# Kernel tuning notes

Hardware: AMD Instinct MI355X
Metric: run time of the kernel (lower is better)

## Reference

```python
import jax, jax.numpy as jnp
import numpy as np
import math

D = 1024
H = 16
FF = 4096
BS = 4
N = 1024
NEG_INF = -jnp.inf


def layer_norm(x, g, b, eps=1e-5):
    mu = jnp.mean(x, axis=-1, keepdims=True)
    var = jnp.var(x, axis=-1, keepdims=True)
    return (x - mu) * jax.lax.rsqrt(var + eps) * g + b


def mha(x, kv, Wq, Wk, Wv, g, b, causal):
    bs, n, d = x.shape
    n_kv = kv.shape[1]
    hd = d // H
    q = (x @ Wq).reshape(bs, n, H, hd)
    k = (kv @ Wk).reshape(bs, n_kv, H, hd)
    v = (kv @ Wv).reshape(bs, n_kv, H, hd)
    # scores scaled by 1/sqrt(model_dim) as in the original (not head_dim!)
    scores = jnp.einsum('bihd,bjhd->bhij', q, k) / math.sqrt(d)
    if causal:
        i = jnp.arange(n)[:, None]
        j = jnp.arange(n_kv)[None, :]
        scores = jnp.where(j <= i, scores, NEG_INF)
    probs = jax.nn.softmax(scores, axis=-1)
    ctx = jnp.einsum('bhij,bjhd->bihd', probs, v).reshape(bs, n, d)
    return layer_norm(ctx + x, g, b)


def setup_inputs() -> dict:
    key = jax.random.key(0)
    ks = jax.random.split(key, 20)
    s_attn = 1.0 / math.sqrt(D)
    s_ff1 = 1.0 / math.sqrt(D)
    s_ff2 = 1.0 / math.sqrt(FF)
    return {
        'x': jax.random.normal(ks[0], (BS, N, D), jnp.float32),
        'encoder_out': jax.random.normal(ks[1], (BS, N, D), jnp.float32),
        'Wq1': jax.random.normal(ks[2], (D, D), jnp.float32) * s_attn,
        'Wk1': jax.random.normal(ks[3], (D, D), jnp.float32) * s_attn,
        'Wv1': jax.random.normal(ks[4], (D, D), jnp.float32) * s_attn,
        'g1': jnp.ones((D,), jnp.float32), 'b1': jnp.zeros((D,), jnp.float32),
        'Wq2': jax.random.normal(ks[5], (D, D), jnp.float32) * s_attn,
        'Wk2': jax.random.normal(ks[6], (D, D), jnp.float32) * s_attn,
        'Wv2': jax.random.normal(ks[7], (D, D), jnp.float32) * s_attn,
        'g2': jnp.ones((D,), jnp.float32), 'b2': jnp.zeros((D,), jnp.float32),
        'W_ff1': jax.random.normal(ks[8], (D, FF), jnp.float32) * s_ff1,
        'b_ff1': jnp.zeros((FF,), jnp.float32),
        'W_ff2': jax.random.normal(ks[9], (FF, D), jnp.float32) * s_ff2,
        'b_ff2': jnp.zeros((D,), jnp.float32),
        'g3': jnp.ones((D,), jnp.float32), 'b3': jnp.zeros((D,), jnp.float32),
    }


def reference(x, encoder_out, Wq1, Wk1, Wv1, g1, b1, Wq2, Wk2, Wv2, g2, b2,
              W_ff1, b_ff1, W_ff2, b_ff2, g3, b3):
    # masked (causal) self-attention
    x = mha(x, x, Wq1, Wk1, Wv1, g1, b1, causal=True)
    # cross-attention over encoder output
    x = mha(x, encoder_out, Wq2, Wk2, Wv2, g2, b2, causal=False)
    # feedforward with exact GELU, residual, layernorm
    h = jax.nn.gelu(x @ W_ff1 + b_ff1, approximate=False)
    out = h @ W_ff2 + b_ff2
    return layer_norm(out + x, g3, b3)
```

## Files before the change

kernel.cpp:

```cpp
#include <hip/hip_runtime.h>

typedef unsigned short u16;
typedef short bf16x8 __attribute__((ext_vector_type(8)));
typedef float f32x4 __attribute__((ext_vector_type(4)));
typedef unsigned short u16x8 __attribute__((ext_vector_type(8)));
typedef unsigned short u16x4 __attribute__((ext_vector_type(4)));

__device__ __forceinline__ u16 f2bf(float f) {
  unsigned u = __builtin_bit_cast(unsigned, f);
  u += 0x7fffu + ((u >> 16) & 1u);
  return (u16)(u >> 16);
}
__device__ __forceinline__ float bf2f(u16 v) {
  return __builtin_bit_cast(float, (unsigned)v << 16);
}

__device__ __forceinline__ void gload_lds16(const void* g, void* l) {
  __builtin_amdgcn_global_load_lds(
      (const __attribute__((address_space(1))) unsigned int*)g,
      (__attribute__((address_space(3))) unsigned int*)l, 16, 0, 0);
}

__global__ __launch_bounds__(256) void cast2_bf16_kernel(const float* __restrict__ s0,
                                                         u16* __restrict__ d0,
                                                         const float* __restrict__ s1,
                                                         u16* __restrict__ d1) {
  const float* s = blockIdx.y ? s1 : s0;
  u16* d = blockIdx.y ? d1 : d0;
  const size_t i = (size_t)blockIdx.x * 256 + threadIdx.x;
  const float4 a = ((const float4*)s)[2 * i];
  const float4 b = ((const float4*)s)[2 * i + 1];
  u16x8 o;
  o[0] = f2bf(a.x); o[1] = f2bf(a.y); o[2] = f2bf(a.z); o[3] = f2bf(a.w);
  o[4] = f2bf(b.x); o[5] = f2bf(b.y); o[6] = f2bf(b.z); o[7] = f2bf(b.w);
  ((u16x8*)d)[i] = o;
}

__global__ __launch_bounds__(256) void pack_bt3_kernel(const float* __restrict__ W0,
                                                       const float* __restrict__ W1,
                                                       const float* __restrict__ W2,
                                                       u16* __restrict__ Bt,
                                                       int K, int N) {
  const float* W = blockIdx.z == 0 ? W0 : (blockIdx.z == 1 ? W1 : W2);
  u16* dst0 = Bt + (size_t)blockIdx.z * K * N;
  __shared__ u16 sh[64][72];
  const int n0 = blockIdx.x * 64, k0 = blockIdx.y * 64;
  const int t = threadIdx.x;
  {
    const int kloc = t >> 2, nc = (t & 3) * 16;
    const float* src = W + (size_t)(k0 + kloc) * N + n0 + nc;
#pragma unroll
    for (int i = 0; i < 16; ++i) sh[kloc][nc + i] = f2bf(src[i]);
  }
  __syncthreads();
  {
    const int nloc = t >> 2, kc = (t & 3) * 16;
    u16 tmp[16];
#pragma unroll
    for (int i = 0; i < 16; ++i) tmp[i] = sh[kc + i][nloc];
    u16* dst = dst0 + (size_t)(n0 + nloc) * K + k0 + kc;
    *(u16x8*)dst = *(const u16x8*)tmp;
    *(u16x8*)(dst + 8) = *(const u16x8*)(tmp + 8);
  }
}

__global__ __launch_bounds__(256) void pack_bt_kernel(const float* __restrict__ W,
                                                      u16* __restrict__ Bt,
                                                      int K, int N) {
  __shared__ u16 sh[64][72];
  const int n0 = blockIdx.x * 64, k0 = blockIdx.y * 64;
  const int t = threadIdx.x;
  {
    const int kloc = t >> 2, nc = (t & 3) * 16;
    const float* src = W + (size_t)(k0 + kloc) * N + n0 + nc;
#pragma unroll
    for (int i = 0; i < 16; ++i) sh[kloc][nc + i] = f2bf(src[i]);
  }
  __syncthreads();
  {
    const int nloc = t >> 2, kc = (t & 3) * 16;
    u16 tmp[16];
#pragma unroll
    for (int i = 0; i < 16; ++i) tmp[i] = sh[kc + i][nloc];
    u16* dst = Bt + (size_t)(n0 + nloc) * K + k0 + kc;
    *(u16x8*)dst = *(const u16x8*)tmp;
    *(u16x8*)(dst + 8) = *(const u16x8*)(tmp + 8);
  }
}

__global__ __launch_bounds__(256) void transpose_v_kernel(const u16* __restrict__ Vsrc,
                                                          u16* __restrict__ Vt,
                                                          int stride) {
  __shared__ u16 sh[64][72];
  const int nt = blockIdx.x;
  const int bh = blockIdx.y;
  const int b = bh >> 4, h = bh & 15;
  const int t = threadIdx.x;
  {
    const int nloc = t >> 2, dc = (t & 3) * 16;
    const u16* src = Vsrc + (size_t)(b * 1024 + nt * 64 + nloc) * stride + h * 64 + dc;
#pragma unroll
    for (int i = 0; i < 16; ++i) sh[nloc][dc + i] = src[i];
  }
  __syncthreads();
  {
    const int dloc = t >> 2, nc = (t & 3) * 16;
    u16 tmp[16];
#pragma unroll
    for (int i = 0; i < 16; ++i) tmp[i] = sh[nc + i][dloc];
    u16* dst = Vt + ((size_t)bh * 64 + dloc) * 1024 + nt * 64 + nc;
    *(u16x8*)dst = *(const u16x8*)tmp;
    *(u16x8*)(dst + 8) = *(const u16x8*)(tmp + 8);
  }
}

template <int EPI>
__global__ __launch_bounds__(512, 4) void gemm_bt(const u16* __restrict__ A,
                                                  const u16* __restrict__ Bt,
                                                  void* __restrict__ Cout,
                                                  const float* __restrict__ bias,
                                                  int M, int N, int K, int lda, int ldb) {
  __shared__ u16 lds[2][2][128 * 64];
  const int tid = threadIdx.x;
  const int lane = tid & 63;
  const int wid = tid >> 6;
  const int wr = wid >> 2;
  const int wc = wid & 3;
  const int g = lane >> 4, cc = lane & 15;
  const int nb = N >> 7;
  const int nwg = gridDim.x;
  const int cpx = nwg >> 3;
  const int bid = (blockIdx.x & 7) * cpx + (blockIdx.x >> 3);
  const int bm = bid / nb, bn = bid % nb;
  const size_t arow0 = (size_t)bm << 7;
  const size_t brow0 = (size_t)bn << 7;
  const size_t koff = (size_t)blockIdx.y * K;

  const u16* ap[2];
  const u16* bp[2];
  int ldst[2];
#pragma unroll
  for (int i = 0; i < 2; ++i) {
    const int tt = i * 512 + tid;
    const int row = tt >> 3;
    const int sc8 = ((tt & 7) ^ (row & 7)) * 8;
    ap[i] = A + (arow0 + row) * lda + koff + sc8;
    bp[i] = Bt + (brow0 + row) * ldb + koff + sc8;
    ldst[i] = (i * 512 + wid * 64) * 8;
  }

  int aoff[4], boff[2];
#pragma unroll
  for (int m = 0; m < 4; ++m) {
    const int rowa = wr * 64 + m * 16 + cc;
    aoff[m] = rowa * 128 + ((g ^ (rowa & 7)) << 4);
  }
#pragma unroll
  for (int n = 0; n < 2; ++n) {
    const int rowb = wc * 32 + n * 16 + cc;
    boff[n] = rowb * 128 + ((g ^ (rowb & 7)) << 4);
  }

  f32x4 acc[4][2] = {};
  const int nk = K >> 6;

#pragma unroll
  for (int i = 0; i < 2; ++i) {
    gload_lds16(ap[i], &lds[0][0][ldst[i]]);
    gload_lds16(bp[i], &lds[0][1][ldst[i]]);
    ap[i] += 64;
    bp[i] += 64;
  }
  __syncthreads();

  int cur = 0;
  for (int kk = 0; kk < nk; ++kk) {
    if (kk + 1 < nk) {
#pragma unroll
      for (int i = 0; i < 2; ++i) {
        gload_lds16(ap[i], &lds[cur ^ 1][0][ldst[i]]);
        gload_lds16(bp[i], &lds[cur ^ 1][1][ldst[i]]);
        ap[i] += 64;
        bp[i] += 64;
      }
    }
    const char* Al = (const char*)&lds[cur][0][0];
    const char* Bl = (const char*)&lds[cur][1][0];
    __builtin_amdgcn_s_setprio(1);
#pragma unroll
    for (int ks = 0; ks < 2; ++ks) {
      const int xr = ks << 6;
      bf16x8 af[4], bfr[2];
#pragma unroll
      for (int m = 0; m < 4; ++m)
        af[m] = *(const bf16x8*)(Al + (aoff[m] ^ xr));
#pragma unroll
      for (int n = 0; n < 2; ++n)
        bfr[n] = *(const bf16x8*)(Bl + (boff[n] ^ xr));
#pragma unroll
      for (int m = 0; m < 4; ++m)
#pragma unroll
        for (int n = 0; n < 2; ++n)
          acc[m][n] = __builtin_amdgcn_mfma_f32_16x16x32_bf16(af[m], bfr[n],
                                                              acc[m][n], 0, 0, 0);
    }
    __builtin_amdgcn_s_setprio(0);
    __syncthreads();
    cur ^= 1;
  }

  const size_t pout = (size_t)blockIdx.y * M * N;
#pragma unroll
  for (int m = 0; m < 4; ++m) {
    const size_t gr0 = arow0 + wr * 64 + m * 16 + (g << 2);
#pragma unroll
    for (int n = 0; n < 2; ++n) {
      const size_t gc = brow0 + wc * 32 + n * 16 + cc;
      float bv = 0.f;
      if constexpr (EPI == 1 || EPI == 2) bv = bias[gc];
#pragma unroll
      for (int r = 0; r < 4; ++r) {
        float v = acc[m][n][r] + bv;
        const size_t idx = (gr0 + r) * (size_t)N + gc;
        if constexpr (EPI == 1) {
          const float u2 = 1.5957691216f * (v + 0.044715f * v * v * v);
          const float e = __expf(u2);
          v = v * e / (e + 1.f);
          ((u16*)Cout)[idx] = f2bf(v);
        } else if constexpr (EPI == 0) {
          ((u16*)Cout)[idx] = f2bf(v);
        } else if constexpr (EPI == 2) {
          ((float*)Cout)[idx] = v;
        } else {
          ((float*)Cout)[pout + idx] = v;
        }
      }
    }
  }
}

template <int CAUSAL>
__global__ __launch_bounds__(256, 6) void attn_kernel(const u16* __restrict__ Qb,
                                                      const u16* __restrict__ Kb,
                                                      const u16* __restrict__ Vt,
                                                      u16* __restrict__ Opart,
                                                      float* __restrict__ lpart,
                                                      int qstride, int kstride) {
  const int qt = blockIdx.x;
  const int bh = blockIdx.y;
  const int z = blockIdx.z;
  const int b = bh >> 4, h = bh & 15;
  const int lane = threadIdx.x & 63;
  const int w = threadIdx.x >> 6;
  const int g = lane >> 4, c = lane & 15;
  const int qbase = qt * 64 + w * 16;

  u16* Op = Opart + (size_t)z * 4096 * 1024;
  float* lp = lpart + (size_t)z * 64 * 1024 + (size_t)bh * 1024;

  int kt0 = z * 8, kt1 = z * 8 + 8;
  if (CAUSAL) kt1 = min(kt1, qt + 1);

  if (kt1 <= kt0) {
#pragma unroll
    for (int r = 0; r < 4; ++r) {
      const int qrow = qbase + g * 4 + r;
      u16x4 zz = {0, 0, 0, 0};
      *(u16x4*)&Op[(size_t)(b * 1024 + qrow) * 1024 + h * 64 + c * 4] = zz;
      if (c == 0) lp[qrow] = 0.f;
    }
    return;
  }

  bf16x8 qf0, qf1;
  {
    const int qrow = qbase + c;
    const u16* qp = Qb + (size_t)(b * 1024 + qrow) * qstride + h * 64 + g * 8;
    qf0 = *(const bf16x8*)qp;
    qf1 = *(const bf16x8*)(qp + 32);
  }

  float l_part[4] = {0.f, 0.f, 0.f, 0.f};
  f32x4 oacc[4] = {};

  __shared__ u16 Kl[64 * 64];
  __shared__ u16 Vl[64 * 64];
  __shared__ u16 Pl[4][16 * 72];
  u16* pw = &Pl[w][0];
  const int tid = threadIdx.x;

  for (int kt = kt0; kt < kt1; ++kt) {
    const int kv0 = kt * 64;
    __syncthreads();
#pragma unroll
    for (int i = 0; i < 2; ++i) {
      const int tt = i * 256 + tid;
      const int row = tt >> 3;
      const int sc = (tt & 7) ^ (row & 7);
      gload_lds16(Kb + (size_t)(b * 1024 + kv0 + row) * kstride + h * 64 + sc * 8,
                  &Kl[(size_t)(i * 256 + w * 64) * 8]);
      gload_lds16(Vt + ((size_t)bh * 64 + row) * 1024 + kv0 + sc * 8,
                  &Vl[(size_t)(i * 256 + w * 64) * 8]);
    }
    __syncthreads();

    f32x4 sacc[4] = {};
#pragma unroll
    for (int t = 0; t < 4; ++t) {
      const int row = t * 16 + c;
      const bf16x8 kf0 = *(const bf16x8*)&Kl[row * 64 + (g ^ (row & 7)) * 8];
      const bf16x8 kf1 = *(const bf16x8*)&Kl[row * 64 + ((4 + g) ^ (row & 7)) * 8];
      sacc[t] = __builtin_amdgcn_mfma_f32_16x16x32_bf16(qf0, kf0, sacc[t], 0, 0, 0);
      sacc[t] = __builtin_amdgcn_mfma_f32_16x16x32_bf16(qf1, kf1, sacc[t], 0, 0, 0);
    }
    const int qr0 = qbase + g * 4;
#pragma unroll
    for (int t = 0; t < 4; ++t) {
      const int kvcol = kv0 + t * 16 + c;
      const int col = t * 16 + c;
#pragma unroll
      for (int r = 0; r < 4; ++r) {
        float p = __expf(sacc[t][r] * 0.03125f);
        if (CAUSAL && kvcol > qr0 + r) p = 0.f;
        l_part[r] += p;
        pw[(g * 4 + r) * 72 + col] = f2bf(p);
      }
    }
#pragma unroll
    for (int ks = 0; ks < 2; ++ks) {
      const bf16x8 pa = *(const bf16x8*)&pw[c * 72 + ks * 32 + g * 8];
#pragma unroll
      for (int t2 = 0; t2 < 4; ++t2) {
        const int row = t2 * 16 + c;
        const bf16x8 vb =
            *(const bf16x8*)&Vl[row * 64 + ((ks * 4 + g) ^ (row & 7)) * 8];
        oacc[t2] = __builtin_amdgcn_mfma_f32_16x16x32_bf16(pa, vb, oacc[t2], 0, 0, 0);
      }
    }
  }
#pragma unroll
  for (int xm = 1; xm < 16; xm <<= 1)
#pragma unroll
    for (int r = 0; r < 4; ++r) l_part[r] += __shfl_xor(l_part[r], xm);
  if (c == 0) {
#pragma unroll
    for (int r = 0; r < 4; ++r) lp[qbase + g * 4 + r] = l_part[r];
  }
#pragma unroll
  for (int t2 = 0; t2 < 4; ++t2) {
    const int d = t2 * 16 + c;
#pragma unroll
    for (int r = 0; r < 4; ++r) {
      const int qrow = qbase + g * 4 + r;
      Op[(size_t)(b * 1024 + qrow) * 1024 + h * 64 + d] = f2bf(oacc[t2][r]);
    }
  }
}

template <int WRITE_BF, int MODE>
__global__ __launch_bounds__(256) void add_ln_kernel(const void* __restrict__ a,
                                                     const float* __restrict__ lpart,
                                                     const float* __restrict__ res,
                                                     const float* __restrict__ gam,
                                                     const float* __restrict__ bet,
                                                     float* __restrict__ yf,
                                                     u16* __restrict__ ybf,
                                                     const float* __restrict__ bias) {
  const size_t row = blockIdx.x;
  const int t = threadIdx.x;
  float x[4];
  if constexpr (MODE == 1) {
    const u16* Ob = (const u16*)a;
    const u16x4 p0 = ((const u16x4*)(Ob + row * 1024))[t];
    const u16x4 p1 = ((const u16x4*)(Ob + (size_t)4096 * 1024 + row * 1024))[t];
    const int b = (int)(row >> 10), q = (int)(row & 1023);
    const int h = t >> 4;
    const size_t li = (size_t)(b * 16 + h) * 1024 + q;
    const float inv = 1.f / (lpart[li] + lpart[(size_t)64 * 1024 + li]);
#pragma unroll
    for (int i = 0; i < 4; ++i) x[i] = (bf2f(p0[i]) + bf2f(p1[i])) * inv;
  } else {
    const float* af = (const float*)a;
    float4 av = ((const float4*)(af + row * 1024))[t];
    if constexpr (MODE == 2) {
      const float4 a2 = ((const float4*)(af + (size_t)4096 * 1024 + row * 1024))[t];
      const float4 bv2 = ((const float4*)bias)[t];
      av.x += a2.x + bv2.x; av.y += a2.y + bv2.y;
      av.z += a2.z + bv2.z; av.w += a2.w + bv2.w;
    }
    x[0] = av.x; x[1] = av.y; x[2] = av.z; x[3] = av.w;
  }
  const float4 rv = ((const float4*)(res + row * 1024))[t];
  x[0] += rv.x; x[1] += rv.y; x[2] += rv.z; x[3] += rv.w;
  float s = x[0] + x[1] + x[2] + x[3];
  float q2 = x[0] * x[0] + x[1] * x[1] + x[2] * x[2] + x[3] * x[3];
#pragma unroll
  for (int m = 1; m < 64; m <<= 1) { s += __shfl_xor(s, m); q2 += __shfl_xor(q2, m); }
  __shared__ float ss[4], sq[4];
  const int w = t >> 6;
  if ((t & 63) == 0) { ss[w] = s; sq[w] = q2; }
  __syncthreads();
  s = ss[0] + ss[1] + ss[2] + ss[3];
  q2 = sq[0] + sq[1] + sq[2] + sq[3];
  const float mu = s * (1.f / 1024.f);
  const float var = q2 * (1.f / 1024.f) - mu * mu;
  const float rstd = rsqrtf(var + 1e-5f);
  const float4 gv = ((const float4*)gam)[t];
  const float4 bv = ((const float4*)bet)[t];
  float y[4];
  y[0] = (x[0] - mu) * rstd * gv.x + bv.x;
  y[1] = (x[1] - mu) * rstd * gv.y + bv.y;
  y[2] = (x[2] - mu) * rstd * gv.z + bv.z;
  y[3] = (x[3] - mu) * rstd * gv.w + bv.w;
  float4 o; o.x = y[0]; o.y = y[1]; o.z = y[2]; o.w = y[3];
  ((float4*)(yf + row * 1024))[t] = o;
  if constexpr (WRITE_BF) {
    u16x4 ob;
    ob[0] = f2bf(y[0]); ob[1] = f2bf(y[1]); ob[2] = f2bf(y[2]); ob[3] = f2bf(y[3]);
    ((u16x4*)(ybf + row * 1024))[t] = ob;
  }
}

extern "C" void kernel_launch(void* const* d_in, const int* in_sizes, int n_in,
                              void* d_out, int out_size, void* d_ws, size_t ws_size,
                              hipStream_t stream) {
  const float* x    = (const float*)d_in[0];
  const float* enc  = (const float*)d_in[1];
  const float* Wq1  = (const float*)d_in[2];
  const float* Wk1  = (const float*)d_in[3];
  const float* Wv1  = (const float*)d_in[4];
  const float* g1   = (const float*)d_in[5];
  const float* b1   = (const float*)d_in[6];
  const float* Wq2  = (const float*)d_in[7];
  const float* Wk2  = (const float*)d_in[8];
  const float* Wv2  = (const float*)d_in[9];
  const float* g2   = (const float*)d_in[10];
  const float* b2   = (const float*)d_in[11];
  const float* Wff1 = (const float*)d_in[12];
  const float* bff1 = (const float*)d_in[13];
  const float* Wff2 = (const float*)d_in[14];
  const float* bff2 = (const float*)d_in[15];
  const float* g3   = (const float*)d_in[16];
  const float* b3   = (const float*)d_in[17];
  float* out = (float*)d_out;

  char* ws = (char*)d_ws;
  const size_t MB = 1024ull * 1024ull;
  u16*   bt  = (u16*)(ws + 0 * MB);
  u16*   big = (u16*)(ws + 8 * MB);
  u16*   vt  = (u16*)(ws + 40 * MB);
  float* ctx = (float*)(ws + 48 * MB);
  float* y1f = (float*)(ws + 64 * MB);
  float* y2f = (float*)(ws + 80 * MB);
  u16*   abf = (u16*)(ws + 96 * MB);
  u16*   ebf = (u16*)(ws + 104 * MB);
  u16*   opart = (u16*)ctx;
  float* lpart = (float*)bt;
  (void)in_sizes; (void)n_in; (void)out_size; (void)ws_size;

  cast2_bf16_kernel<<<dim3(2048, 2), 256, 0, stream>>>(x, abf, enc, ebf);

  pack_bt3_kernel<<<dim3(16, 16, 3), 256, 0, stream>>>(Wq1, Wk1, Wv1, bt, 1024, 1024);
  gemm_bt<0><<<(4096 / 128) * (3072 / 128), 512, 0, stream>>>(abf, bt, big, nullptr,
                                                              4096, 3072, 1024, 1024, 1024);
  transpose_v_kernel<<<dim3(16, 64), 256, 0, stream>>>(big + 2048, vt, 3072);
  attn_kernel<1><<<dim3(16, 64, 2), 256, 0, stream>>>(big, big + 1024, vt, opart, lpart,
                                                      3072, 3072);
  add_ln_kernel<1, 1><<<4096, 256, 0, stream>>>(opart, lpart, x, g1, b1, y1f, abf, nullptr);

  pack_bt3_kernel<<<dim3(16, 16, 3), 256, 0, stream>>>(Wq2, Wk2, Wv2, bt, 1024, 1024);
  u16* q2  = big;
  u16* kv2 = big + (size_t)4096 * 1024;
  gemm_bt<0><<<(4096 / 128) * (1024 / 128), 512, 0, stream>>>(abf, bt, q2, nullptr,
                                                              4096, 1024, 1024, 1024, 1024);
  gemm_bt<0><<<(4096 / 128) * (2048 / 128), 512, 0, stream>>>(ebf, bt + (size_t)1024 * 1024,
                                                              kv2, nullptr, 4096, 2048, 1024,
                                                              1024, 1024);
  transpose_v_kernel<<<dim3(16, 64), 256, 0, stream>>>(kv2 + 1024, vt, 2048);
  attn_kernel<0><<<dim3(16, 64, 2), 256, 0, stream>>>(q2, kv2, vt, opart, lpart, 1024, 2048);
  add_ln_kernel<1, 1><<<4096, 256, 0, stream>>>(opart, lpart, y1f, g2, b2, y2f, abf, nullptr);

  pack_bt_kernel<<<dim3(64, 16), 256, 0, stream>>>(Wff1, bt, 1024, 4096);
  gemm_bt<1><<<(4096 / 128) * (4096 / 128), 512, 0, stream>>>(abf, bt, big, bff1,
                                                              4096, 4096, 1024, 1024, 1024);
  pack_bt_kernel<<<dim3(16, 64), 256, 0, stream>>>(Wff2, bt, 4096, 1024);
  gemm_bt<3><<<dim3((4096 / 128) * (1024 / 128), 2), 512, 0, stream>>>(big, bt, ctx, nullptr,
                                                                       4096, 1024, 2048,
                                                                       4096, 4096);
  add_ln_kernel<0, 2><<<4096, 256, 0, stream>>>(ctx, nullptr, y2f, g3, b3, out, nullptr, bff2);
}
```

Measured before the change: 291.6 us.

## Fuse V transpose into QKV GEMM epilogue and carry residuals in bf16

The QKV and KV projection GEMMs now write the V columns directly in transposed per-head layout, which removes both transpose_v kernel launches and their extra read/write of V. The layernorm kernels stop writing fp32 copies of the intermediate activations and instead take the bf16 activation buffer as the residual input. This cuts memory traffic, but the residuals now carry bf16 precision instead of fp32. The layernorm for the second attention reads and writes the same abf buffer in place. The transposed V stores are 4-element strided writes, which may coalesce poorly.

Measured after the change: 282.4 us. 3.2% less time.

```diff
diff --git a/kernel.cpp b/kernel.cpp
--- a/kernel.cpp
+++ b/kernel.cpp
@@ -88,37 +88,12 @@
   }
 }
 
-__global__ __launch_bounds__(256) void transpose_v_kernel(const u16* __restrict__ Vsrc,
-                                                          u16* __restrict__ Vt,
-                                                          int stride) {
-  __shared__ u16 sh[64][72];
-  const int nt = blockIdx.x;
-  const int bh = blockIdx.y;
-  const int b = bh >> 4, h = bh & 15;
-  const int t = threadIdx.x;
-  {
-    const int nloc = t >> 2, dc = (t & 3) * 16;
-    const u16* src = Vsrc + (size_t)(b * 1024 + nt * 64 + nloc) * stride + h * 64 + dc;
-#pragma unroll
-    for (int i = 0; i < 16; ++i) sh[nloc][dc + i] = src[i];
-  }
-  __syncthreads();
-  {
-    const int dloc = t >> 2, nc = (t & 3) * 16;
-    u16 tmp[16];
-#pragma unroll
-    for (int i = 0; i < 16; ++i) tmp[i] = sh[nc + i][dloc];
-    u16* dst = Vt + ((size_t)bh * 64 + dloc) * 1024 + nt * 64 + nc;
-    *(u16x8*)dst = *(const u16x8*)tmp;
-    *(u16x8*)(dst + 8) = *(const u16x8*)(tmp + 8);
-  }
-}
-
-template <int EPI>
+template <int EPI, int VOUT>
 __global__ __launch_bounds__(512, 4) void gemm_bt(const u16* __restrict__ A,
                                                   const u16* __restrict__ Bt,
                                                   void* __restrict__ Cout,
                                                   const float* __restrict__ bias,
+                                                  u16* __restrict__ vt, int voff,
                                                   int M, int N, int K, int lda, int ldb) {
   __shared__ u16 lds[2][2][128 * 64];
   const int tid = threadIdx.x;
@@ -216,8 +191,18 @@
 #pragma unroll
     for (int n = 0; n < 2; ++n) {
       const size_t gc = brow0 + wc * 32 + n * 16 + cc;
+      if (VOUT && (int)gc >= voff) {
+        const int col = (int)gc - voff;
+        const int hh = col >> 6, dd = col & 63;
+        const int bb = (int)(gr0 >> 10), nn = (int)(gr0 & 1023);
+        u16x4 ov;
+#pragma unroll
+        for (int r = 0; r < 4; ++r) ov[r] = f2bf(acc[m][n][r]);
+        *(u16x4*)&vt[(((size_t)(bb * 16 + hh) * 64 + dd) << 10) + nn] = ov;
+        continue;
+      }
       float bv = 0.f;
-      if constexpr (EPI == 1 || EPI == 2) bv = bias[gc];
+      if constexpr (EPI == 1) bv = bias[gc];
 #pragma unroll
       for (int r = 0; r < 4; ++r) {
         float v = acc[m][n][r] + bv;
@@ -229,8 +214,6 @@
           ((u16*)Cout)[idx] = f2bf(v);
         } else if constexpr (EPI == 0) {
           ((u16*)Cout)[idx] = f2bf(v);
-        } else if constexpr (EPI == 2) {
-          ((float*)Cout)[idx] = v;
         } else {
           ((float*)Cout)[pout + idx] = v;
         }
@@ -357,10 +340,10 @@
   }
 }
 
-template <int WRITE_BF, int MODE>
+template <int MODE, int RES_BF, int OUT_F>
 __global__ __launch_bounds__(256) void add_ln_kernel(const void* __restrict__ a,
                                                      const float* __restrict__ lpart,
-                                                     const float* __restrict__ res,
+                                                     const void* __restrict__ res,
                                                      const float* __restrict__ gam,
                                                      const float* __restrict__ bet,
                                                      float* __restrict__ yf,
@@ -382,16 +365,19 @@
   } else {
     const float* af = (const float*)a;
     float4 av = ((const float4*)(af + row * 1024))[t];
-    if constexpr (MODE == 2) {
-      const float4 a2 = ((const float4*)(af + (size_t)4096 * 1024 + row * 1024))[t];
-      const float4 bv2 = ((const float4*)bias)[t];
-      av.x += a2.x + bv2.x; av.y += a2.y + bv2.y;
-      av.z += a2.z + bv2.z; av.w += a2.w + bv2.w;
-    }
-    x[0] = av.x; x[1] = av.y; x[2] = av.z; x[3] = av.w;
-  }
-  const float4 rv = ((const float4*)(res + row * 1024))[t];
-  x[0] += rv.x; x[1] += rv.y; x[2] += rv.z; x[3] += rv.w;
+    const float4 a2 = ((const float4*)(af + (size_t)4096 * 1024 + row * 1024))[t];
+    const float4 bv2 = ((const float4*)bias)[t];
+    x[0] = av.x + a2.x + bv2.x; x[1] = av.y + a2.y + bv2.y;
+    x[2] = av.z + a2.z + bv2.z; x[3] = av.w + a2.w + bv2.w;
+  }
+  if constexpr (RES_BF) {
+    const u16x4 rv = ((const u16x4*)((const u16*)res + row * 1024))[t];
+#pragma unroll
+    for (int i = 0; i < 4; ++i) x[i] += bf2f(rv[i]);
+  } else {
+    const float4 rv = ((const float4*)((const float*)res + row * 1024))[t];
+    x[0] += rv.x; x[1] += rv.y; x[2] += rv.z; x[3] += rv.w;
+  }
   float s = x[0] + x[1] + x[2] + x[3];
   float q2 = x[0] * x[0] + x[1] * x[1] + x[2] * x[2] + x[3] * x[3];
 #pragma unroll
@@ -412,9 +398,10 @@
   y[1] = (x[1] - mu) * rstd * gv.y + bv.y;
   y[2] = (x[2] - mu) * rstd * gv.z + bv.z;
   y[3] = (x[3] - mu) * rstd * gv.w + bv.w;
-  float4 o; o.x = y[0]; o.y = y[1]; o.z = y[2]; o.w = y[3];
-  ((float4*)(yf + row * 1024))[t] = o;
-  if constexpr (WRITE_BF) {
+  if constexpr (OUT_F) {
+    float4 o; o.x = y[0]; o.y = y[1]; o.z = y[2]; o.w = y[3];
+    ((float4*)(yf + row * 1024))[t] = o;
+  } else {
     u16x4 ob;
     ob[0] = f2bf(y[0]); ob[1] = f2bf(y[1]); ob[2] = f2bf(y[2]); ob[3] = f2bf(y[3]);
     ((u16x4*)(ybf + row * 1024))[t] = ob;
@@ -450,8 +437,7 @@
   u16*   big = (u16*)(ws + 8 * MB);
   u16*   vt  = (u16*)(ws + 40 * MB);
   float* ctx = (float*)(ws + 48 * MB);
-  float* y1f = (float*)(ws + 64 * MB);
-  float* y2f = (float*)(ws + 80 * MB);
+  float* p1f = (float*)(ws + 64 * MB);
   u16*   abf = (u16*)(ws + 96 * MB);
   u16*   ebf = (u16*)(ws + 104 * MB);
   u16*   opart = (u16*)ctx;
@@ -461,31 +447,30 @@
   cast2_bf16_kernel<<<dim3(2048, 2), 256, 0, stream>>>(x, abf, enc, ebf);
 
   pack_bt3_kernel<<<dim3(16, 16, 3), 256, 0, stream>>>(Wq1, Wk1, Wv1, bt, 1024, 1024);
-  gemm_bt<0><<<(4096 / 128) * (3072 / 128), 512, 0, stream>>>(abf, bt, big, nullptr,
-                                                              4096, 3072, 1024, 1024, 1024);
-  transpose_v_kernel<<<dim3(16, 64), 256, 0, stream>>>(big + 2048, vt, 3072);
+  gemm_bt<0, 1><<<(4096 / 128) * (3072 / 128), 512, 0, stream>>>(
+      abf, bt, big, nullptr, vt, 2048, 4096, 3072, 1024, 1024, 1024);
   attn_kernel<1><<<dim3(16, 64, 2), 256, 0, stream>>>(big, big + 1024, vt, opart, lpart,
                                                       3072, 3072);
-  add_ln_kernel<1, 1><<<4096, 256, 0, stream>>>(opart, lpart, x, g1, b1, y1f, abf, nullptr);
+  add_ln_kernel<1, 0, 0><<<4096, 256, 0, stream>>>(opart, lpart, x, g1, b1,
+                                                   nullptr, abf, nullptr);
 
   pack_bt3_kernel<<<dim3(16, 16, 3), 256, 0, stream>>>(Wq2, Wk2, Wv2, bt, 1024, 1024);
   u16* q2  = big;
   u16* kv2 = big + (size_t)4096 * 1024;
-  gemm_bt<0><<<(4096 / 128) * (1024 / 128), 512, 0, stream>>>(abf, bt, q2, nullptr,
-                                                              4096, 1024, 1024, 1024, 1024);
-  gemm_bt<0><<<(4096 / 128) * (2048 / 128), 512, 0, stream>>>(ebf, bt + (size_t)1024 * 1024,
-                                                              kv2, nullptr, 4096, 2048, 1024,
-                                                              1024, 1024);
-  transpose_v_kernel<<<dim3(16, 64), 256, 0, stream>>>(kv2 + 1024, vt, 2048);
+  gemm_bt<0, 0><<<(4096 / 128) * (1024 / 128), 512, 0, stream>>>(
+      abf, bt, q2, nullptr, nullptr, 0, 4096, 1024, 1024, 1024, 1024);
+  gemm_bt<0, 1><<<(4096 / 128) * (2048 / 128), 512, 0, stream>>>(
+      ebf, bt + (size_t)1024 * 1024, kv2, nullptr, vt, 1024, 4096, 2048, 1024, 1024, 1024);
   attn_kernel<0><<<dim3(16, 64, 2), 256, 0, stream>>>(q2, kv2, vt, opart, lpart, 1024, 2048);
-  add_ln_kernel<1, 1><<<4096, 256, 0, stream>>>(opart, lpart, y1f, g2, b2, y2f, abf, nullptr);
+  add_ln_kernel<1, 1, 0><<<4096, 256, 0, stream>>>(opart, lpart, abf, g2, b2,
+                                                   nullptr, abf, nullptr);
 
   pack_bt_kernel<<<dim3(64, 16), 256, 0, stream>>>(Wff1, bt, 1024, 4096);
-  gemm_bt<1><<<(4096 / 128) * (4096 / 128), 512, 0, stream>>>(abf, bt, big, bff1,
-                                                              4096, 4096, 1024, 1024, 1024);
+  gemm_bt<1, 0><<<(4096 / 128) * (4096 / 128), 512, 0, stream>>>(
+      abf, bt, big, bff1, nullptr, 0, 4096, 4096, 1024, 1024, 1024);
   pack_bt_kernel<<<dim3(16, 64), 256, 0, stream>>>(Wff2, bt, 4096, 1024);
-  gemm_bt<3><<<dim3((4096 / 128) * (1024 / 128), 2), 512, 0, stream>>>(big, bt, ctx, nullptr,
-                                                                       4096, 1024, 2048,
-                                                                       4096, 4096);
-  add_ln_kernel<0, 2><<<4096, 256, 0, stream>>>(ctx, nullptr, y2f, g3, b3, out, nullptr, bff2);
-}
+  gemm_bt<3, 0><<<dim3((4096 / 128) * (1024 / 128), 2), 512, 0, stream>>>(
+      big, bt, ctx, nullptr, nullptr, 0, 4096, 1024, 2048, 4096, 4096);
+  add_ln_kernel<2, 1, 1><<<4096, 256, 0, stream>>>(ctx, nullptr, abf, g3, b3,
+                                                   out, nullptr, bff2);
+}
```
